# Performance work log

Measured on AMD Instinct MI355X. Metric: run time of the kernel, lower is better.

The kernel has to match this reference:

```python
import jax, jax.numpy as jnp
import numpy as np

DIM = 128


def conv2d(x, w, b=None, pad=0, groups=1):
    y = jax.lax.conv_general_dilated(
        x, w, window_strides=(1, 1), padding=[(pad, pad), (pad, pad)],
        dimension_numbers=('NCHW', 'OIHW', 'NCHW'), feature_group_count=groups)
    if b is not None:
        y = y + b[None, :, None, None]
    return y


def min_gru(x, w):
    # x: (B, H, W, V, C); linear recurrence along V (axis -2).
    # minGRU: z = sigmoid(gate), h_tilde = g(hidden), h_t = (1-z_t)h_{t-1} + z_t h_tilde_t
    hg = jnp.einsum('bhwvc,dc->bhwvd', x, w)  # Linear(dim -> 2*dim, no bias)
    hidden, gate = jnp.split(hg, 2, axis=-1)
    z = jax.nn.sigmoid(gate)
    h_tilde = jnp.where(hidden >= 0, hidden + 0.5, jax.nn.sigmoid(hidden))
    a = 1.0 - z
    b = z * h_tilde

    def combine(c1, c2):
        a1, b1 = c1
        a2, b2 = c2
        return a1 * a2, b1 * a2 + b2

    _, h = jax.lax.associative_scan(combine, (a, b), axis=-2)
    return h


def pixel_shuffle(x, r):
    B, C, H, W = x.shape
    c = C // (r * r)
    x = x.reshape(B, c, r, r, H, W).transpose(0, 1, 4, 2, 5, 3)
    return x.reshape(B, c, H * r, W * r)


def setup_inputs():
    key = jax.random.key(0)
    ks = jax.random.split(key, 16)
    B, V, C, H, W = 2, 6, DIM, 128, 128
    s = 0.02
    return {
        'feats': jax.random.normal(ks[0], (B, V, C, H, W), jnp.float32),
        'prj_feats': jax.random.normal(ks[1], (B, V, C, H, W), jnp.float32),
        'merge_w1': jax.random.normal(ks[2], (C, 2 * C, 1, 1), jnp.float32) * s,
        'merge_b1': jnp.zeros((C,), jnp.float32),
        'merge_wd': jax.random.normal(ks[3], (C, 1, 3, 3), jnp.float32) * s,
        'merge_bd': jnp.zeros((C,), jnp.float32),
        'merge_w2': jax.random.normal(ks[4], (C, C, 1, 1), jnp.float32) * s,
        'merge_b2': jnp.zeros((C,), jnp.float32),
        'gru_w': jax.random.normal(ks[5], (2 * C, C), jnp.float32) * s,
        'gru_back_w': jax.random.normal(ks[6], (2 * C, C), jnp.float32) * s,
        'alpha_w': jax.random.normal(ks[7], (1, C, 3, 3), jnp.float32) * s,
        'alpha_b': jnp.zeros((1,), jnp.float32),
        'up_w': jax.random.normal(ks[8], (C, C, 1, 1), jnp.float32) * s,
        'up_b': jnp.zeros((C,), jnp.float32),
        'outc_w': jax.random.normal(ks[9], (3, C // 16, 3, 3), jnp.float32) * s,
        'outc_b': jnp.zeros((3,), jnp.float32),
        'oh': 512,
        'ow': 512,
    }


def reference(feats, prj_feats, merge_w1, merge_b1, merge_wd, merge_bd,
              merge_w2, merge_b2, gru_w, gru_back_w, alpha_w, alpha_b,
              up_w, up_b, outc_w, outc_b, oh, ow):
    B, V, C, H, W = prj_feats.shape
    f = feats.reshape(B * V, C, H, W)
    p = prj_feats.reshape(B * V, C, H, W)
    # merge: 1x1 conv -> GELU -> depthwise 3x3 -> GELU -> 1x1 conv, residual add
    m = conv2d(jnp.concatenate([f, p], axis=1), merge_w1, merge_b1)
    m = jax.nn.gelu(m, approximate=False)
    m = conv2d(m, merge_wd, merge_bd, pad=1, groups=C)
    m = jax.nn.gelu(m, approximate=False)
    m = conv2d(m, merge_w2, merge_b2)
    f = f + m
    # bidirectional minGRU over the view axis
    f = f.reshape(B, V, C, H, W).transpose(0, 3, 4, 1, 2)  # (B,H,W,V,C)
    f = min_gru(f, gru_w)
    f = jnp.flip(f, axis=1)  # faithful to torch.flip(dims=[1])
    f = min_gru(f, gru_back_w)
    f = jnp.flip(f, axis=1)
    f = f.transpose(0, 3, 4, 1, 2).reshape(B * V, C, H, W)
    # softmax view-attention pooling
    alpha = conv2d(f, alpha_w, alpha_b, pad=1).reshape(B, V, 1, H, W)
    f = jnp.sum(f.reshape(B, V, C, H, W) * jax.nn.softmax(alpha, axis=1), axis=1)
    # pixel-shuffle upsampler (x4: dim -> dim//16) + resize to original_shape
    u = conv2d(f, up_w, up_b)
    u = pixel_shuffle(u, 4)  # (B, C//16, 4H, 4W)
    u = jax.image.resize(u, (B, C // 16, oh, ow), method='bilinear')
    return conv2d(u, outc_w, outc_b, pad=1)
```

## Files before the change

kernel.cpp:

```cpp
#include <hip/hip_runtime.h>


#define DEV static __device__ __forceinline__

typedef __attribute__((ext_vector_type(8))) short short8x;
typedef __attribute__((ext_vector_type(4))) float f32x4;

constexpr int Bc = 2, Vc = 6, Cc = 128, Hc = 128, Wc = 128;
constexpr int Nc = Bc * Vc;
constexpr int Pc = Hc * Wc;
constexpr int NPX = Nc * Pc;

DEV float us2f(unsigned short u) {
  return __builtin_bit_cast(float, (unsigned int)u << 16);
}
DEV unsigned short f2us(float f) {
  unsigned int i = __builtin_bit_cast(unsigned int, f);
  unsigned int r = i + 0x7FFFu + ((i >> 16) & 1u);
  return (unsigned short)(r >> 16);
}
DEV float geluf(float x) { return x * 0.5f * (1.f + erff(x * 0.70710678118654752f)); }
DEV float sigm(float x) { return 1.f / (1.f + __expf(-x)); }

__global__ __launch_bounds__(256) void k_prepw(
    const float* __restrict__ w1, const float* __restrict__ w2,
    const float* __restrict__ wu, const float* __restrict__ gw,
    const float* __restrict__ gbw, unsigned short* __restrict__ wbf) {
  int idx = blockIdx.x * 256 + threadIdx.x;
  float v;
  if (idx < 32768) {
    v = w1[idx];
  } else if (idx < 49152) {
    v = w2[idx - 32768];
  } else if (idx < 65536) {
    v = wu[idx - 49152];
  } else {
    int i = (idx < 98304) ? (idx - 65536) : (idx - 98304);
    int np = i >> 7, k = i & 127;
    int j = np >> 5, s = np & 31;
    int src = (s < 16) ? (16 * j + s) : (128 + 16 * j + (s - 16));
    const float* w = (idx < 98304) ? gw : gbw;
    v = w[src * 128 + k];
  }
  wbf[idx] = f2us(v);
}

__global__ __launch_bounds__(256) void k_merge1(
    const float* __restrict__ feats, const float* __restrict__ prj,
    const unsigned short* __restrict__ w1b, const float* __restrict__ b1,
    unsigned short* __restrict__ m1, unsigned short* __restrict__ fres) {
  __shared__ unsigned short sA[64][72];
  const int t = threadIdx.x;
  const int wave = t >> 6, lane = t & 63, quad = lane >> 4, lr = lane & 15;
  const int mb = blockIdx.x;
  const int n = mb >> 8;
  const int p0 = (mb & 255) << 6;
  const size_t m0 = (size_t)n * Pc + p0;
  const int px = t & 63;
  const int ho = t >> 6;
  const int wn2 = wave * 32;

  f32x4 acc[4][2];
#pragma unroll
  for (int i = 0; i < 4; i++)
#pragma unroll
    for (int j = 0; j < 2; j++) acc[i][j] = (f32x4){0.f, 0.f, 0.f, 0.f};

#pragma unroll 1
  for (int s = 0; s < 4; ++s) {
    const int k0 = s * 64;
    float ra[2][8];
#pragma unroll
    for (int g = 0; g < 2; ++g) {
      const int ch = k0 + ho * 16 + g * 8;
      const float* src = (ch < 128)
          ? (feats + (size_t)(n * 128 + ch) * Pc)
          : (prj + (size_t)(n * 128 + (ch - 128)) * Pc);
      src += p0 + px;
#pragma unroll
      for (int j = 0; j < 8; ++j) ra[g][j] = src[(size_t)j * Pc];
    }
    __syncthreads();
#pragma unroll
    for (int g = 0; g < 2; ++g) {
      unsigned int pk[4];
#pragma unroll
      for (int q2 = 0; q2 < 4; ++q2)
        pk[q2] = (unsigned int)f2us(ra[g][2 * q2]) |
                 ((unsigned int)f2us(ra[g][2 * q2 + 1]) << 16);
      uint4 w4;
      w4.x = pk[0]; w4.y = pk[1]; w4.z = pk[2]; w4.w = pk[3];
      *(uint4*)&sA[px][ho * 16 + g * 8] = w4;
    }
    __syncthreads();
    short8x bf2[2][2];
#pragma unroll
    for (int ks = 0; ks < 2; ++ks)
#pragma unroll
      for (int j = 0; j < 2; j++)
        bf2[ks][j] = *reinterpret_cast<const short8x*>(
            w1b + (size_t)(wn2 + j * 16 + lr) * 256 + k0 + ks * 32 + quad * 8);
#pragma unroll
    for (int ks = 0; ks < 2; ++ks) {
      const int kk = ks * 32 + quad * 8;
      short8x a[4];
#pragma unroll
      for (int i = 0; i < 4; i++)
        a[i] = *reinterpret_cast<const short8x*>(&sA[i * 16 + lr][kk]);
#pragma unroll
      for (int i = 0; i < 4; i++)
#pragma unroll
        for (int j = 0; j < 2; j++)
          acc[i][j] = __builtin_amdgcn_mfma_f32_16x16x32_bf16(a[i], bf2[ks][j], acc[i][j], 0, 0, 0);
    }
    if (k0 < 128) {
      for (int u = t; u < 512; u += 256) {
        int row = u >> 3, seg = u & 7;
        *(uint4*)(fres + (m0 + row) * 128 + k0 + seg * 8) =
            *(const uint4*)&sA[row][seg * 8];
      }
    }
  }
#pragma unroll
  for (int i = 0; i < 4; i++)
#pragma unroll
    for (int r = 0; r < 4; r++) {
      size_t row = m0 + i * 16 + quad * 4 + r;
#pragma unroll
      for (int j = 0; j < 2; j++) {
        int c = wn2 + j * 16 + lr;
        m1[row * 128 + c] = f2us(geluf(acc[i][j][r] + b1[c]));
      }
    }
}

__global__ __launch_bounds__(256) void k_dw(
    const unsigned short* __restrict__ in, const float* __restrict__ wd,
    const float* __restrict__ bd, unsigned short* __restrict__ out) {
  __shared__ float w[Cc * 9];
  for (int i = threadIdx.x; i < Cc * 9; i += 256) w[i] = wd[i];
  __syncthreads();
  const int wave = threadIdx.x >> 6, lane = threadIdx.x & 63;
  const int gid = blockIdx.x * 4 + wave;
  const int n = gid >> 12, p4 = (gid & 4095) << 2;
  const int y = p4 >> 7, x0 = p4 & 127;
  const int c0 = 2 * lane;
  const float* w0 = w + c0 * 9;
  const float* w1 = w + (c0 + 1) * 9;
  float a0[4], a1[4];
#pragma unroll
  for (int k = 0; k < 4; ++k) { a0[k] = bd[c0]; a1[k] = bd[c0 + 1]; }
#pragma unroll
  for (int dy = 0; dy < 3; ++dy) {
    int yy = y + dy - 1;
    if (yy < 0 || yy >= Hc) continue;
    const unsigned short* rowp = in + ((size_t)(n * Pc + yy * Wc)) * 128 + c0;
    float tx[6], ty[6];
#pragma unroll
    for (int j = 0; j < 6; ++j) {
      int xx = x0 + j - 1;
      if (xx >= 0 && xx < Wc) {
        ushort2 v = *(const ushort2*)(rowp + (size_t)xx * 128);
        tx[j] = us2f(v.x); ty[j] = us2f(v.y);
      } else { tx[j] = 0.f; ty[j] = 0.f; }
    }
#pragma unroll
    for (int k = 0; k < 4; ++k)
#pragma unroll
      for (int dx = 0; dx < 3; ++dx) {
        a0[k] += w0[dy * 3 + dx] * tx[k + dx];
        a1[k] += w1[dy * 3 + dx] * ty[k + dx];
      }
  }
#pragma unroll
  for (int k = 0; k < 4; ++k) {
    ushort2 pk;
    pk.x = f2us(geluf(a0[k]));
    pk.y = f2us(geluf(a1[k]));
    *(ushort2*)(out + ((size_t)(n * Pc) + p4 + k) * 128 + c0) = pk;
  }
}

__global__ __launch_bounds__(256) void k_merge2(
    const unsigned short* __restrict__ A, const unsigned short* __restrict__ w2b,
    const float* __restrict__ b2, const unsigned short* __restrict__ fres,
    unsigned short* __restrict__ X1) {
  __shared__ unsigned short sA[128][72];
  __shared__ unsigned short sB[128][72];
  const int t = threadIdx.x;
  const int wave = t >> 6, lane = t & 63, quad = lane >> 4, lr = lane & 15;
  const int wm = (wave >> 1) * 64, wn = (wave & 1) * 64;
  const size_t m0 = (size_t)blockIdx.x * 128;
  f32x4 acc[4][4];
#pragma unroll
  for (int i = 0; i < 4; i++)
#pragma unroll
    for (int j = 0; j < 4; j++) acc[i][j] = (f32x4){0.f, 0.f, 0.f, 0.f};

  for (int k0 = 0; k0 < 128; k0 += 64) {
    for (int u = t; u < 1024; u += 256) {
      int row = u >> 3, seg = u & 7;
      *(uint4*)&sA[row][seg * 8] =
          *(const uint4*)(A + (m0 + row) * 128 + k0 + seg * 8);
    }
    for (int u = t; u < 1024; u += 256) {
      int row = u >> 3, seg = u & 7;
      *(uint4*)&sB[row][seg * 8] =
          *(const uint4*)(w2b + (size_t)row * 128 + k0 + seg * 8);
    }
    __syncthreads();
#pragma unroll
    for (int ks = 0; ks < 2; ++ks) {
      const int kk = ks * 32 + quad * 8;
      short8x a[4], bf[4];
#pragma unroll
      for (int i = 0; i < 4; i++)
        a[i] = *reinterpret_cast<const short8x*>(&sA[wm + i * 16 + lr][kk]);
#pragma unroll
      for (int j = 0; j < 4; j++)
        bf[j] = *reinterpret_cast<const short8x*>(&sB[wn + j * 16 + lr][kk]);
#pragma unroll
      for (int i = 0; i < 4; i++)
#pragma unroll
        for (int j = 0; j < 4; j++)
          acc[i][j] = __builtin_amdgcn_mfma_f32_16x16x32_bf16(a[i], bf[j], acc[i][j], 0, 0, 0);
    }
    __syncthreads();
  }
#pragma unroll
  for (int i = 0; i < 4; i++)
#pragma unroll
    for (int r = 0; r < 4; r++) {
      size_t row = m0 + wm + i * 16 + quad * 4 + r;
#pragma unroll
      for (int j = 0; j < 4; j++) {
        int c = wn + j * 16 + lr;
        float v = acc[i][j][r] + b2[c] + us2f(fres[row * 128 + c]);
        X1[row * 128 + c] = f2us(v);
      }
    }
}

__global__ __launch_bounds__(512) void k_gru(
    const unsigned short* __restrict__ X1, const unsigned short* __restrict__ Wg,
    const unsigned short* __restrict__ Wb, unsigned short* __restrict__ F2) {
  __shared__ unsigned short sA[96][72];
  __shared__ unsigned short sH[96][136];
  const int t = threadIdx.x;
  const int wave = t >> 6, lane = t & 63, quad = lane >> 4, lr = lane & 15;
  const int blk = blockIdx.x;
  const int b = blk >> 10, p0 = (blk & 1023) << 4;
  f32x4 acc[6][2];
#pragma unroll
  for (int v = 0; v < 6; v++)
#pragma unroll
    for (int j = 0; j < 2; j++) acc[v][j] = (f32x4){0.f, 0.f, 0.f, 0.f};

#pragma unroll 1
  for (int k0 = 0; k0 < 128; k0 += 64) {
    __syncthreads();
    for (int u = t; u < 768; u += 512) {
      int r = u >> 3, seg = u & 7;
      int v = r >> 4, ps = r & 15;
      *(uint4*)&sA[r][seg * 8] =
          *(const uint4*)(X1 + ((size_t)((b * 6 + v) * Pc + p0 + ps)) * 128 + k0 + seg * 8);
    }
    __syncthreads();
#pragma unroll
    for (int ks = 0; ks < 2; ++ks) {
      const int kk = ks * 32 + quad * 8;
      short8x a[6], bf[2];
#pragma unroll
      for (int j = 0; j < 2; j++)
        bf[j] = *reinterpret_cast<const short8x*>(
            Wg + (size_t)(wave * 32 + j * 16 + lr) * 128 + k0 + kk);
#pragma unroll
      for (int v = 0; v < 6; v++)
        a[v] = *reinterpret_cast<const short8x*>(&sA[v * 16 + lr][kk]);
#pragma unroll
      for (int v = 0; v < 6; v++)
#pragma unroll
        for (int j = 0; j < 2; j++)
          acc[v][j] = __builtin_amdgcn_mfma_f32_16x16x32_bf16(a[v], bf[j], acc[v][j], 0, 0, 0);
    }
  }
  __syncthreads();
#pragma unroll
  for (int r = 0; r < 4; r++) {
    float h = 0.f;
#pragma unroll
    for (int v = 0; v < 6; v++) {
      float hid = acc[v][0][r], gat = acc[v][1][r];
      float z = sigm(gat);
      float ht = (hid >= 0.f) ? (hid + 0.5f) : sigm(hid);
      h = (1.f - z) * h + z * ht;
      sH[v * 16 + quad * 4 + r][wave * 16 + lr] = f2us(h);
    }
  }
  __syncthreads();

#pragma unroll
  for (int v = 0; v < 6; v++)
#pragma unroll
    for (int j = 0; j < 2; j++) acc[v][j] = (f32x4){0.f, 0.f, 0.f, 0.f};
#pragma unroll 1
  for (int k0 = 0; k0 < 128; k0 += 64) {
#pragma unroll
    for (int ks = 0; ks < 2; ++ks) {
      const int kk = ks * 32 + quad * 8;
      short8x a[6], bf[2];
#pragma unroll
      for (int j = 0; j < 2; j++)
        bf[j] = *reinterpret_cast<const short8x*>(
            Wb + (size_t)(wave * 32 + j * 16 + lr) * 128 + k0 + kk);
#pragma unroll
      for (int v = 0; v < 6; v++)
        a[v] = *reinterpret_cast<const short8x*>(&sH[v * 16 + lr][k0 + kk]);
#pragma unroll
      for (int v = 0; v < 6; v++)
#pragma unroll
        for (int j = 0; j < 2; j++)
          acc[v][j] = __builtin_amdgcn_mfma_f32_16x16x32_bf16(a[v], bf[j], acc[v][j], 0, 0, 0);
    }
  }
#pragma unroll
  for (int r = 0; r < 4; r++) {
    float h = 0.f;
#pragma unroll
    for (int v = 0; v < 6; v++) {
      float hid = acc[v][0][r], gat = acc[v][1][r];
      float z = sigm(gat);
      float ht = (hid >= 0.f) ? (hid + 0.5f) : sigm(hid);
      h = (1.f - z) * h + z * ht;
      F2[((size_t)((b * 6 + v) * Pc + p0 + quad * 4 + r)) * 128 + wave * 16 + lr] =
          f2us(h);
    }
  }
}

__global__ __launch_bounds__(256) void k_apool(
    const unsigned short* __restrict__ F, const float* __restrict__ wa,
    const float* __restrict__ ba, unsigned short* __restrict__ P2) {
  __shared__ float w[Cc * 9];
  for (int i = threadIdx.x; i < Cc * 9; i += 256) w[i] = wa[i];
  __syncthreads();
  const int wave = threadIdx.x >> 6, lane = threadIdx.x & 63;
  const int px = blockIdx.x * 4 + wave;
  const int b = px >> 14, p = px & (Pc - 1);
  const int y = p >> 7, x = p & 127;
  const int c0 = 2 * lane;
  const float* w0 = w + c0 * 9;
  const float* w1 = w + (c0 + 1) * 9;
  float av[Vc];
  ushort2 ctr[Vc];
#pragma unroll
  for (int v = 0; v < Vc; ++v) {
    const unsigned short* Fv = F + ((size_t)((b * Vc + v) * Pc)) * 128;
    float acc = 0.f;
#pragma unroll
    for (int dy = 0; dy < 3; ++dy) {
      int yy = y + dy - 1;
      if (yy < 0 || yy >= Hc) continue;
#pragma unroll
      for (int dx = 0; dx < 3; ++dx) {
        int xx = x + dx - 1;
        if (xx < 0 || xx >= Wc) continue;
        const unsigned short* row = Fv + ((size_t)(yy * Wc + xx)) * 128;
        ushort2 vv = *(const ushort2*)(row + c0);
        if (dy == 1 && dx == 1) ctr[v] = vv;
        acc += w0[dy * 3 + dx] * us2f(vv.x) + w1[dy * 3 + dx] * us2f(vv.y);
      }
    }
#pragma unroll
    for (int off = 32; off >= 1; off >>= 1) acc += __shfl_xor(acc, off);
    av[v] = acc + ba[0];
  }
  float mx = -1e30f;
#pragma unroll
  for (int v = 0; v < Vc; ++v) mx = fmaxf(mx, av[v]);
  float s = 0.f;
#pragma unroll
  for (int v = 0; v < Vc; ++v) { av[v] = __expf(av[v] - mx); s += av[v]; }
  const float inv = 1.f / s;
  float a0 = 0.f, a1 = 0.f;
#pragma unroll
  for (int v = 0; v < Vc; ++v) {
    float sw = av[v] * inv;
    a0 += us2f(ctr[v].x) * sw;
    a1 += us2f(ctr[v].y) * sw;
  }
  ushort2 pk;
  pk.x = f2us(a0);
  pk.y = f2us(a1);
  *(ushort2*)(P2 + (size_t)px * 128 + c0) = pk;
}

__global__ __launch_bounds__(256) void k_up(
    const unsigned short* __restrict__ A, const unsigned short* __restrict__ wub,
    const float* __restrict__ bu, unsigned short* __restrict__ us_) {
  __shared__ unsigned short sA[128][72];
  __shared__ unsigned short sB[128][72];
  const int t = threadIdx.x;
  const int wave = t >> 6, lane = t & 63, quad = lane >> 4, lr = lane & 15;
  const int wm = (wave >> 1) * 64, wn = (wave & 1) * 64;
  const size_t m0 = (size_t)blockIdx.x * 128;
  f32x4 acc[4][4];
#pragma unroll
  for (int i = 0; i < 4; i++)
#pragma unroll
    for (int j = 0; j < 4; j++) acc[i][j] = (f32x4){0.f, 0.f, 0.f, 0.f};

  for (int k0 = 0; k0 < 128; k0 += 64) {
    for (int u = t; u < 1024; u += 256) {
      int row = u >> 3, seg = u & 7;
      *(uint4*)&sA[row][seg * 8] =
          *(const uint4*)(A + (m0 + row) * 128 + k0 + seg * 8);
    }
    for (int u = t; u < 1024; u += 256) {
      int row = u >> 3, seg = u & 7;
      *(uint4*)&sB[row][seg * 8] =
          *(const uint4*)(wub + (size_t)row * 128 + k0 + seg * 8);
    }
    __syncthreads();
#pragma unroll
    for (int ks = 0; ks < 2; ++ks) {
      const int kk = ks * 32 + quad * 8;
      short8x a[4], bf[4];
#pragma unroll
      for (int i = 0; i < 4; i++)
        a[i] = *reinterpret_cast<const short8x*>(&sA[wm + i * 16 + lr][kk]);
#pragma unroll
      for (int j = 0; j < 4; j++)
        bf[j] = *reinterpret_cast<const short8x*>(&sB[wn + j * 16 + lr][kk]);
#pragma unroll
      for (int i = 0; i < 4; i++)
#pragma unroll
        for (int j = 0; j < 4; j++)
          acc[i][j] = __builtin_amdgcn_mfma_f32_16x16x32_bf16(a[i], bf[j], acc[i][j], 0, 0, 0);
    }
    __syncthreads();
  }
#pragma unroll
  for (int i = 0; i < 4; i++)
#pragma unroll
    for (int r = 0; r < 4; r++) {
      size_t row = m0 + wm + i * 16 + quad * 4 + r;
      int b = (int)(row >> 14), p = (int)(row & (Pc - 1));
      int y = p >> 7, x = p & 127;
#pragma unroll
      for (int j = 0; j < 4; j++) {
        int c = wn + j * 16 + lr;
        float v = acc[i][j][r] + bu[c];
        int co = c >> 4, r1 = (c >> 2) & 3, r2 = c & 3;
        us_[(((size_t)b * 8 + co) * 512 + (y * 4 + r1)) * 512 + (x * 4 + r2)] = f2us(v);
      }
    }
}

__global__ __launch_bounds__(256) void k_outc(
    const unsigned short* __restrict__ us_, const float* __restrict__ wo,
    const float* __restrict__ bo, float* __restrict__ out) {
  __shared__ float w[3 * 8 * 9];
  for (int i = threadIdx.x; i < 216; i += 256) w[i] = wo[i];
  __syncthreads();
  int i = blockIdx.x;
  const int xh = i & 1; i >>= 1;
  const int Y = i & 511; i >>= 9;
  const int b = i;
  const int X = xh * 256 + threadIdx.x;
  float a0 = bo[0], a1 = bo[1], a2 = bo[2];
  for (int ci = 0; ci < 8; ++ci) {
    const unsigned short* pl = us_ + ((size_t)b * 8 + ci) * 512 * 512;
    const float* w0 = w + 0 * 72 + ci * 9;
    const float* w1 = w + 1 * 72 + ci * 9;
    const float* w2 = w + 2 * 72 + ci * 9;
#pragma unroll
    for (int dy = 0; dy < 3; ++dy) {
      int YY = Y + dy - 1;
      if (YY < 0 || YY >= 512) continue;
#pragma unroll
      for (int dx = 0; dx < 3; ++dx) {
        int XX = X + dx - 1;
        if (XX < 0 || XX >= 512) continue;
        float v = us2f(pl[(size_t)YY * 512 + XX]);
        a0 += w0[dy * 3 + dx] * v;
        a1 += w1[dy * 3 + dx] * v;
        a2 += w2[dy * 3 + dx] * v;
      }
    }
  }
  out[(((size_t)b * 3 + 0) * 512 + Y) * 512 + X] = a0;
  out[(((size_t)b * 3 + 1) * 512 + Y) * 512 + X] = a1;
  out[(((size_t)b * 3 + 2) * 512 + Y) * 512 + X] = a2;
}

extern "C" void kernel_launch(void* const* d_in, const int* in_sizes, int n_in,
                              void* d_out, int out_size, void* d_ws, size_t ws_size,
                              hipStream_t stream) {
  const float* feats = (const float*)d_in[0];
  const float* prj = (const float*)d_in[1];
  const float* w1 = (const float*)d_in[2];
  const float* b1 = (const float*)d_in[3];
  const float* wd = (const float*)d_in[4];
  const float* bd = (const float*)d_in[5];
  const float* w2 = (const float*)d_in[6];
  const float* b2 = (const float*)d_in[7];
  const float* gw = (const float*)d_in[8];
  const float* gbw = (const float*)d_in[9];
  const float* wa = (const float*)d_in[10];
  const float* ba = (const float*)d_in[11];
  const float* wu = (const float*)d_in[12];
  const float* bu = (const float*)d_in[13];
  const float* wo = (const float*)d_in[14];
  const float* bo = (const float*)d_in[15];
  float* out = (float*)d_out;

  char* ws = (char*)d_ws;
  unsigned short* buf0 = (unsigned short*)(ws + 0);
  unsigned short* buf1 = (unsigned short*)(ws + 50331648);
  unsigned short* fres = (unsigned short*)(ws + 100663296);
  unsigned short* P2 = (unsigned short*)(ws + 151781376);
  unsigned short* ushuf = (unsigned short*)(ws + 160169984);
  unsigned short* wbf = (unsigned short*)(ws + 168558592);

  const unsigned short* w1b = wbf;
  const unsigned short* w2b = wbf + 32768;
  const unsigned short* wub = wbf + 49152;
  const unsigned short* wgi = wbf + 65536;
  const unsigned short* wgbi = wbf + 98304;

  dim3 blk(256);
  k_prepw<<<dim3(512), blk, 0, stream>>>(w1, w2, wu, gw, gbw, wbf);
  k_merge1<<<dim3(NPX / 64), blk, 0, stream>>>(feats, prj, w1b, b1, buf0, fres);
  k_dw<<<dim3(NPX / 16), blk, 0, stream>>>(buf0, wd, bd, buf1);
  k_merge2<<<dim3(NPX / 128), blk, 0, stream>>>(buf1, w2b, b2, fres, buf0);
  k_gru<<<dim3(Bc * (Pc / 16)), dim3(512), 0, stream>>>(buf0, wgi, wgbi, buf1);
  k_apool<<<dim3(Bc * Pc / 4), blk, 0, stream>>>(buf1, wa, ba, P2);
  k_up<<<dim3(Bc * Pc / 128), blk, 0, stream>>>(P2, wub, bu, ushuf);
  k_outc<<<dim3(2 * 512 * 2), blk, 0, stream>>>(ushuf, wo, bo, out);

  (void)in_sizes; (void)n_in; (void)out_size; (void)ws_size;
}
```

Measured before the change: 565.0 us.

## Fuse depthwise 3x3 conv+GELU into the second 1x1 merge GEMM

Replaces the separate depthwise-conv kernel and the merge2 GEMM with one kernel. Each block computes depthwise conv plus GELU for 64 pixels into shared memory and feeds that tile straight into MFMA against w2, adding bias and the residual. This removes the round trip of the intermediate activation tensor through global memory and one launch. In exchange, B weights are read from global/cache per wave without LDS staging, and each block recomputes over halo rows.

```diff
diff --git a/kernel.cpp b/kernel.cpp
--- a/kernel.cpp
+++ b/kernel.cpp
@@ -134,107 +134,109 @@
     }
 }
 
-__global__ __launch_bounds__(256) void k_dw(
-    const unsigned short* __restrict__ in, const float* __restrict__ wd,
-    const float* __restrict__ bd, unsigned short* __restrict__ out) {
-  __shared__ float w[Cc * 9];
-  for (int i = threadIdx.x; i < Cc * 9; i += 256) w[i] = wd[i];
-  __syncthreads();
-  const int wave = threadIdx.x >> 6, lane = threadIdx.x & 63;
-  const int gid = blockIdx.x * 4 + wave;
-  const int n = gid >> 12, p4 = (gid & 4095) << 2;
-  const int y = p4 >> 7, x0 = p4 & 127;
-  const int c0 = 2 * lane;
-  const float* w0 = w + c0 * 9;
-  const float* w1 = w + (c0 + 1) * 9;
-  float a0[4], a1[4];
-#pragma unroll
-  for (int k = 0; k < 4; ++k) { a0[k] = bd[c0]; a1[k] = bd[c0 + 1]; }
-#pragma unroll
-  for (int dy = 0; dy < 3; ++dy) {
-    int yy = y + dy - 1;
-    if (yy < 0 || yy >= Hc) continue;
-    const unsigned short* rowp = in + ((size_t)(n * Pc + yy * Wc)) * 128 + c0;
-    float tx[6], ty[6];
-#pragma unroll
-    for (int j = 0; j < 6; ++j) {
-      int xx = x0 + j - 1;
-      if (xx >= 0 && xx < Wc) {
-        ushort2 v = *(const ushort2*)(rowp + (size_t)xx * 128);
-        tx[j] = us2f(v.x); ty[j] = us2f(v.y);
-      } else { tx[j] = 0.f; ty[j] = 0.f; }
-    }
-#pragma unroll
-    for (int k = 0; k < 4; ++k)
-#pragma unroll
-      for (int dx = 0; dx < 3; ++dx) {
-        a0[k] += w0[dy * 3 + dx] * tx[k + dx];
-        a1[k] += w1[dy * 3 + dx] * ty[k + dx];
-      }
-  }
-#pragma unroll
-  for (int k = 0; k < 4; ++k) {
-    ushort2 pk;
-    pk.x = f2us(geluf(a0[k]));
-    pk.y = f2us(geluf(a1[k]));
-    *(ushort2*)(out + ((size_t)(n * Pc) + p4 + k) * 128 + c0) = pk;
-  }
-}
-
-__global__ __launch_bounds__(256) void k_merge2(
-    const unsigned short* __restrict__ A, const unsigned short* __restrict__ w2b,
+__global__ __launch_bounds__(256) void k_dwm2(
+    const unsigned short* __restrict__ m1, const float* __restrict__ wd,
+    const float* __restrict__ bd, const unsigned short* __restrict__ w2b,
     const float* __restrict__ b2, const unsigned short* __restrict__ fres,
     unsigned short* __restrict__ X1) {
-  __shared__ unsigned short sA[128][72];
-  __shared__ unsigned short sB[128][72];
+  __shared__ unsigned short sA[64][72];
+  __shared__ float wdt[9 * 128];
+  __shared__ float bds[128];
   const int t = threadIdx.x;
   const int wave = t >> 6, lane = t & 63, quad = lane >> 4, lr = lane & 15;
-  const int wm = (wave >> 1) * 64, wn = (wave & 1) * 64;
-  const size_t m0 = (size_t)blockIdx.x * 128;
-  f32x4 acc[4][4];
+  const int mb = blockIdx.x;
+  const int n = mb >> 8;
+  const int p0 = (mb & 255) << 6;
+  const size_t m0 = (size_t)n * Pc + p0;
+  const int y = p0 >> 7, xbase = p0 & 127;
+  const int wn2 = wave * 32;
+
+  for (int i = t; i < 1152; i += 256) {
+    int ch = i / 9, tap = i - ch * 9;
+    wdt[tap * 128 + ch] = wd[i];
+  }
+  for (int i = t; i < 128; i += 256) bds[i] = bd[i];
+  __syncthreads();
+
+  {
+    const int oct = t & 15, pxq = t >> 4;
+    const int ch0 = oct * 8;
+    float acc8[4][8];
+#pragma unroll
+    for (int p = 0; p < 4; ++p)
+#pragma unroll
+      for (int e = 0; e < 8; ++e) acc8[p][e] = bds[ch0 + e];
+#pragma unroll
+    for (int dy = 0; dy < 3; ++dy) {
+      int yy = y + dy - 1;
+      if (yy < 0 || yy >= Hc) continue;
+      const unsigned short* rowp = m1 + ((size_t)(n * Pc + yy * Wc)) * 128 + ch0;
+#pragma unroll
+      for (int dx = 0; dx < 3; ++dx) {
+        float wreg[8];
+        *(float4*)&wreg[0] = *(const float4*)&wdt[(dy * 3 + dx) * 128 + ch0];
+        *(float4*)&wreg[4] = *(const float4*)&wdt[(dy * 3 + dx) * 128 + ch0 + 4];
+#pragma unroll
+        for (int p = 0; p < 4; ++p) {
+          int xx = xbase + pxq * 4 + p + dx - 1;
+          if (xx < 0 || xx >= Wc) continue;
+          short8x v = *reinterpret_cast<const short8x*>(rowp + (size_t)xx * 128);
+#pragma unroll
+          for (int e = 0; e < 8; ++e)
+            acc8[p][e] += wreg[e] * us2f((unsigned short)v[e]);
+        }
+      }
+    }
+#pragma unroll
+    for (int p = 0; p < 4; ++p) {
+      unsigned int pk[4];
+#pragma unroll
+      for (int q2 = 0; q2 < 4; ++q2)
+        pk[q2] = (unsigned int)f2us(geluf(acc8[p][2 * q2])) |
+                 ((unsigned int)f2us(geluf(acc8[p][2 * q2 + 1])) << 16);
+      uint4 w4;
+      w4.x = pk[0]; w4.y = pk[1]; w4.z = pk[2]; w4.w = pk[3];
+      *(uint4*)&sA[pxq * 4 + p][ch0] = w4;
+    }
+  }
+  __syncthreads();
+
+  f32x4 acc[4][2];
 #pragma unroll
   for (int i = 0; i < 4; i++)
 #pragma unroll
-    for (int j = 0; j < 4; j++) acc[i][j] = (f32x4){0.f, 0.f, 0.f, 0.f};
-
+    for (int j = 0; j < 2; j++) acc[i][j] = (f32x4){0.f, 0.f, 0.f, 0.f};
+#pragma unroll
   for (int k0 = 0; k0 < 128; k0 += 64) {
-    for (int u = t; u < 1024; u += 256) {
-      int row = u >> 3, seg = u & 7;
-      *(uint4*)&sA[row][seg * 8] =
-          *(const uint4*)(A + (m0 + row) * 128 + k0 + seg * 8);
-    }
-    for (int u = t; u < 1024; u += 256) {
-      int row = u >> 3, seg = u & 7;
-      *(uint4*)&sB[row][seg * 8] =
-          *(const uint4*)(w2b + (size_t)row * 128 + k0 + seg * 8);
-    }
-    __syncthreads();
+    short8x bf2[2][2];
+#pragma unroll
+    for (int ks = 0; ks < 2; ++ks)
+#pragma unroll
+      for (int j = 0; j < 2; j++)
+        bf2[ks][j] = *reinterpret_cast<const short8x*>(
+            w2b + (size_t)(wn2 + j * 16 + lr) * 128 + k0 + ks * 32 + quad * 8);
 #pragma unroll
     for (int ks = 0; ks < 2; ++ks) {
-      const int kk = ks * 32 + quad * 8;
-      short8x a[4], bf[4];
+      const int kk = k0 + ks * 32 + quad * 8;
+      short8x a[4];
 #pragma unroll
       for (int i = 0; i < 4; i++)
-        a[i] = *reinterpret_cast<const short8x*>(&sA[wm + i * 16 + lr][kk]);
-#pragma unroll
-      for (int j = 0; j < 4; j++)
-        bf[j] = *reinterpret_cast<const short8x*>(&sB[wn + j * 16 + lr][kk]);
+        a[i] = *reinterpret_cast<const short8x*>(&sA[i * 16 + lr][kk]);
 #pragma unroll
       for (int i = 0; i < 4; i++)
 #pragma unroll
-        for (int j = 0; j < 4; j++)
-          acc[i][j] = __builtin_amdgcn_mfma_f32_16x16x32_bf16(a[i], bf[j], acc[i][j], 0, 0, 0);
-    }
-    __syncthreads();
+        for (int j = 0; j < 2; j++)
+          acc[i][j] = __builtin_amdgcn_mfma_f32_16x16x32_bf16(a[i], bf2[ks][j], acc[i][j], 0, 0, 0);
+    }
   }
 #pragma unroll
   for (int i = 0; i < 4; i++)
 #pragma unroll
     for (int r = 0; r < 4; r++) {
-      size_t row = m0 + wm + i * 16 + quad * 4 + r;
-#pragma unroll
-      for (int j = 0; j < 4; j++) {
-        int c = wn + j * 16 + lr;
+      size_t row = m0 + i * 16 + quad * 4 + r;
+#pragma unroll
+      for (int j = 0; j < 2; j++) {
+        int c = wn2 + j * 16 + lr;
         float v = acc[i][j][r] + b2[c] + us2f(fres[row * 128 + c]);
         X1[row * 128 + c] = f2us(v);
       }
@@ -532,10 +534,9 @@
   dim3 blk(256);
   k_prepw<<<dim3(512), blk, 0, stream>>>(w1, w2, wu, gw, gbw, wbf);
   k_merge1<<<dim3(NPX / 64), blk, 0, stream>>>(feats, prj, w1b, b1, buf0, fres);
-  k_dw<<<dim3(NPX / 16), blk, 0, stream>>>(buf0, wd, bd, buf1);
-  k_merge2<<<dim3(NPX / 128), blk, 0, stream>>>(buf1, w2b, b2, fres, buf0);
-  k_gru<<<dim3(Bc * (Pc / 16)), dim3(512), 0, stream>>>(buf0, wgi, wgbi, buf1);
-  k_apool<<<dim3(Bc * Pc / 4), blk, 0, stream>>>(buf1, wa, ba, P2);
+  k_dwm2<<<dim3(NPX / 64), blk, 0, stream>>>(buf0, wd, bd, w2b, b2, fres, buf1);
+  k_gru<<<dim3(Bc * (Pc / 16)), dim3(512), 0, stream>>>(buf1, wgi, wgbi, buf0);
+  k_apool<<<dim3(Bc * Pc / 4), blk, 0, stream>>>(buf0, wa, ba, P2);
   k_up<<<dim3(Bc * Pc / 128), blk, 0, stream>>>(P2, wub, bu, ushuf);
   k_outc<<<dim3(2 * 512 * 2), blk, 0, stream>>>(ushuf, wo, bo, out);
 
```

Result: faster. 539.0 us (-4.6%).
